# Kernel optimization log

Hardware: AMD Instinct MI355X
Metric: run time of the kernel (lower is better)

Reference implementation:

```python
import jax, jax.numpy as jnp
import numpy as np

EPS = 1e-7  # keras_backend.epsilon()
ROUTINGS = 3


def setup_inputs() -> dict:
    key = jax.random.key(0)
    k1, k2, k3, k4, k5 = jax.random.split(key, 5)
    B, H, W, I, O = 32, 8, 8, 32, 64
    return {
        "inputs_poses": jax.random.normal(k1, (B, H, W, I, 4, 4), dtype=jnp.float32),
        "inputs_activations": jax.random.uniform(k2, (B, H, W, I), dtype=jnp.float32),
        "w": jax.random.normal(k3, (I, O, 4, 4), dtype=jnp.float32),
        "beta_v": jax.random.normal(k4, (1, O), dtype=jnp.float32),
        "beta_a": jax.random.normal(k5, (1, O), dtype=jnp.float32),
    }


def _em_routing(votes, i_act, beta_v, beta_a, routings):
    # votes: [B, N, O, 16], i_act: [B, N]
    B, N, O, P = votes.shape
    act = i_act[..., None, None]              # [B, N, 1, 1]
    bv = beta_v[..., None, :, None]           # [1, 1, O, 1]
    ba = beta_a[..., None, :, None]           # [1, 1, O, 1]
    rr = jnp.full((N, O, 1), 1.0 / O, dtype=votes.dtype)
    it_min, it_max = 1.0, min(routings, 3.0)
    o_mean = o_act = None
    for it in range(routings):
        inv_temp = it_min + (it_max - it_min) * it / max(1.0, routings - 1.0)
        # ---- m-step ----
        rr_prime = rr * act                                    # [B, N, O, 1]
        rps = rr_prime.sum(axis=-3, keepdims=True)             # [B, 1, O, 1]
        o_mean = (rr_prime * votes).sum(axis=-3, keepdims=True) / rps   # [B,1,O,16]
        o_stdv = jnp.sqrt((rr_prime * jnp.square(votes - o_mean)).sum(axis=-3, keepdims=True) / rps)
        o_cost_h = (bv + jnp.log(o_stdv + EPS)) * rps          # [B,1,O,16]
        o_cost = o_cost_h.sum(axis=-1, keepdims=True)          # [B,1,O,1]
        o_cost_mean = o_cost.mean(axis=-2, keepdims=True)      # [B,1,1,1]
        o_cost_stdv = jnp.sqrt(jnp.square(o_cost - o_cost_mean).sum(axis=-2, keepdims=True) / O)
        o_act = jax.nn.sigmoid(inv_temp * (ba + (o_cost_mean - o_cost) / (o_cost_stdv + EPS)))
        # ---- e-step ----
        if it < routings - 1:
            o_p = (-jnp.sum(jnp.square(votes - o_mean) / (2.0 * jnp.square(o_stdv)), axis=-1, keepdims=True)
                   - jnp.sum(jnp.log(o_stdv + EPS), axis=-1, keepdims=True))   # [B,N,O,1]
            zz = jnp.log(o_act + EPS) + o_p
            rr = jax.nn.softmax(zz, axis=-2)                   # softmax over O
    poses = jnp.squeeze(o_mean, axis=-3)                       # [B, O, 16]
    activations = jnp.squeeze(o_act, axis=(-3, -1))            # [B, O]
    return poses, activations


def reference(inputs_poses, inputs_activations, w, beta_v, beta_a):
    B, H, W, I = inputs_activations.shape
    O = w.shape[1]
    # mat_transform: per-(input-type, class) 4x4 pose transform -> votes
    pose = inputs_poses.reshape(B * H * W, I, 4, 4)
    votes = jnp.einsum('siab,iobc->sioac', pose, w)            # [BHW, I, O, 4, 4]
    votes = votes.reshape(B, H, W, I, O, 16)
    # coord_addition: add scaled spatial coords to components 0 (h) and 1 (w)
    ch = jnp.zeros((1, H, 1, 1, 1, 16), votes.dtype).at[..., 0].set(
        ((jnp.arange(H, dtype=votes.dtype) + 0.5) / H).reshape(1, H, 1, 1, 1))
    cw = jnp.zeros((1, 1, W, 1, 1, 16), votes.dtype).at[..., 1].set(
        ((jnp.arange(W, dtype=votes.dtype) + 0.5) / W).reshape(1, 1, W, 1, 1))
    votes = votes + ch + cw
    votes = votes.reshape(B, H * W * I, O, 16)
    i_act = inputs_activations.reshape(B, H * W * I)
    poses, activations = _em_routing(votes, i_act, beta_v, beta_a, ROUTINGS)
    poses = poses.reshape(B, O, 4, 4)
    return poses, activations
```

## Files before the change

### kernel.cpp

```cpp
#include <hip/hip_runtime.h>


#define NB 32
#define NN 2048
#define NO 64
#define NP 16
#define EPSF 1e-7f

#define CHUNKS 64
#define CHN 32

#define ACC_SLOTS 33
#define ACC_PER_B (ACC_SLOTS * NO)
#define ACC_TOTAL (NB * ACC_PER_B)

template <bool FIRST>
__global__ __launch_bounds__(256) void accum_kernel(
    const float* __restrict__ pose,
    const float* __restrict__ act,
    const float* __restrict__ wmat,
    const float* __restrict__ beta_v,
    const float* __restrict__ beta_a,
    const float* __restrict__ accum_prev,
    float* __restrict__ accum_out,
    float inv_temp)
{
    __shared__ float pose_s[CHN * 16];
    __shared__ float act_s[CHN];
    __shared__ float red[2][ACC_PER_B];

    const int b = blockIdx.y;
    const int site = blockIdx.x;
    const int n0 = site * CHN;
    const int tid = threadIdx.x;

    {
        const float4* psrc = (const float4*)(pose + ((size_t)b * NN + n0) * 16);
        float4* pdst = (float4*)pose_s;
        if (tid < CHN * 4) pdst[tid] = psrc[tid];
        if (tid < CHN) act_s[tid] = act[(size_t)b * NN + n0 + tid];
    }
    __syncthreads();

    const int wv = tid >> 6;
    const int o = tid & 63;

    float i2v[16], Bp[16], zzc = 0.f;
    if (!FIRST) {
        const float* ap = accum_prev + (size_t)b * ACC_PER_B;
        float rps = ap[32 * 64 + o];
        float rinv = 1.0f / rps;
        float logsum = 0.f, msum = 0.f;
        #pragma unroll
        for (int p = 0; p < 16; p++) {
            float mm = ap[p * 64 + o] * rinv;
            float vv = fmaxf(ap[(16 + p) * 64 + o] * rinv - mm * mm, 0.f);
            float iv = 0.5f / vv;
            i2v[p] = iv;
            Bp[p] = 2.0f * mm * iv;
            msum = fmaf(mm * mm, iv, msum);
            logsum += __logf(sqrtf(vv) + EPSF);
        }
        float cost = rps * (16.0f * beta_v[o] + logsum);
        float cm = cost;
        #pragma unroll
        for (int s = 32; s > 0; s >>= 1) cm += __shfl_xor(cm, s, 64);
        cm *= (1.0f / 64.0f);
        float dd = cost - cm;
        float cs = dd * dd;
        #pragma unroll
        for (int s = 32; s > 0; s >>= 1) cs += __shfl_xor(cs, s, 64);
        cs = sqrtf(cs * (1.0f / 64.0f));
        float x = inv_temp * (beta_a[o] + (cm - cost) / (cs + EPSF));
        float oa = 1.0f / (1.0f + __expf(-x));
        zzc = __logf(oa + EPSF) - logsum - msum;
    }

    const float c0 = ((site >> 3) + 0.5f) * 0.125f;
    const float c1 = ((site & 7) + 0.5f) * 0.125f;

    float accR = 0.f, acc1[16], acc2[16];
    #pragma unroll
    for (int p = 0; p < 16; p++) { acc1[p] = 0.f; acc2[p] = 0.f; }

    for (int ii = 0; ii < 8; ii++) {
        const int i = wv * 8 + ii;
        const float4* wp = (const float4*)(wmat + ((size_t)i * 64 + o) * 16);
        float4 w0 = wp[0], w1 = wp[1], w2 = wp[2], w3 = wp[3];
        const float* pr = pose_s + i * 16;
        float v[16];
        #pragma unroll
        for (int a = 0; a < 4; a++) {
            float pa0 = pr[a * 4 + 0], pa1 = pr[a * 4 + 1];
            float pa2 = pr[a * 4 + 2], pa3 = pr[a * 4 + 3];
            v[a * 4 + 0] = pa0 * w0.x + pa1 * w1.x + pa2 * w2.x + pa3 * w3.x;
            v[a * 4 + 1] = pa0 * w0.y + pa1 * w1.y + pa2 * w2.y + pa3 * w3.y;
            v[a * 4 + 2] = pa0 * w0.z + pa1 * w1.z + pa2 * w2.z + pa3 * w3.z;
            v[a * 4 + 3] = pa0 * w0.w + pa1 * w1.w + pa2 * w2.w + pa3 * w3.w;
        }
        v[0] += c0;
        v[1] += c1;

        float rr;
        if (FIRST) {
            rr = 1.0f / 64.0f;
        } else {
            float d = zzc;
            #pragma unroll
            for (int p = 0; p < 16; p++) {
                float inner = fmaf(-v[p], i2v[p], Bp[p]);
                d = fmaf(v[p], inner, d);
            }
            float mx = d;
            #pragma unroll
            for (int s = 32; s > 0; s >>= 1) mx = fmaxf(mx, __shfl_xor(mx, s, 64));
            float e = __expf(d - mx);
            float sum = e;
            #pragma unroll
            for (int s = 32; s > 0; s >>= 1) sum += __shfl_xor(sum, s, 64);
            rr = __fdividef(e, sum);
        }
        float rp = rr * act_s[i];
        accR += rp;
        #pragma unroll
        for (int p = 0; p < 16; p++) {
            acc1[p] += rp * v[p];
            acc2[p] += rp * v[p] * v[p];
        }
    }

    if (wv >= 2) {
        float* r = red[wv - 2];
        r[32 * 64 + o] = accR;
        #pragma unroll
        for (int p = 0; p < 16; p++) r[p * 64 + o] = acc1[p];
        #pragma unroll
        for (int p = 0; p < 16; p++) r[(16 + p) * 64 + o] = acc2[p];
    }
    __syncthreads();
    if (wv < 2) {
        const float* r = red[wv];
        accR += r[32 * 64 + o];
        #pragma unroll
        for (int p = 0; p < 16; p++) acc1[p] += r[p * 64 + o];
        #pragma unroll
        for (int p = 0; p < 16; p++) acc2[p] += r[(16 + p) * 64 + o];
    }
    __syncthreads();
    if (wv == 1) {
        float* r = red[0];
        r[32 * 64 + o] = accR;
        #pragma unroll
        for (int p = 0; p < 16; p++) r[p * 64 + o] = acc1[p];
        #pragma unroll
        for (int p = 0; p < 16; p++) r[(16 + p) * 64 + o] = acc2[p];
    }
    __syncthreads();
    if (wv == 0) {
        const float* r = red[0];
        accR += r[32 * 64 + o];
        #pragma unroll
        for (int p = 0; p < 16; p++) acc1[p] += r[p * 64 + o];
        #pragma unroll
        for (int p = 0; p < 16; p++) acc2[p] += r[(16 + p) * 64 + o];

        float* ac = accum_out + (size_t)b * ACC_PER_B;
        atomicAdd(ac + 32 * 64 + o, accR);
        #pragma unroll
        for (int p = 0; p < 16; p++) atomicAdd(ac + p * 64 + o, acc1[p]);
        #pragma unroll
        for (int p = 0; p < 16; p++) atomicAdd(ac + (16 + p) * 64 + o, acc2[p]);
    }
}

__global__ __launch_bounds__(64) void stats_final(
    const float* __restrict__ accum,
    const float* __restrict__ beta_v,
    const float* __restrict__ beta_a,
    float* __restrict__ out,
    float inv_temp)
{
    const int b = blockIdx.x;
    const int o = threadIdx.x;
    const float* ac = accum + (size_t)b * ACC_PER_B;

    float rps = ac[32 * 64 + o];
    float rinv = 1.0f / rps;
    float m[16];
    float logsum = 0.f;
    #pragma unroll
    for (int p = 0; p < 16; p++) {
        float mm = ac[p * 64 + o] * rinv;
        float vv = fmaxf(ac[(16 + p) * 64 + o] * rinv - mm * mm, 0.f);
        m[p] = mm;
        logsum += __logf(sqrtf(vv) + EPSF);
    }
    float cost = rps * (16.0f * beta_v[o] + logsum);

    float cm = cost;
    #pragma unroll
    for (int s = 32; s > 0; s >>= 1) cm += __shfl_xor(cm, s, 64);
    cm *= (1.0f / 64.0f);
    float dd = cost - cm;
    float cs = dd * dd;
    #pragma unroll
    for (int s = 32; s > 0; s >>= 1) cs += __shfl_xor(cs, s, 64);
    cs = sqrtf(cs * (1.0f / 64.0f));

    float x = inv_temp * (beta_a[o] + (cm - cost) / (cs + EPSF));
    float oa = 1.0f / (1.0f + __expf(-x));

    float* op = out + ((size_t)b * 64 + o) * 16;
    #pragma unroll
    for (int p = 0; p < 16; p++) op[p] = m[p];
    out[(size_t)NB * NO * NP + (size_t)b * 64 + o] = oa;
}

extern "C" void kernel_launch(void* const* d_in, const int* in_sizes, int n_in,
                              void* d_out, int out_size, void* d_ws, size_t ws_size,
                              hipStream_t stream) {
    const float* pose   = (const float*)d_in[0];
    const float* act    = (const float*)d_in[1];
    const float* wmat   = (const float*)d_in[2];
    const float* beta_v = (const float*)d_in[3];
    const float* beta_a = (const float*)d_in[4];
    float* out = (float*)d_out;
    float* ws = (float*)d_ws;

    float* a0 = ws;
    float* a1 = ws + (size_t)ACC_TOTAL;
    float* a2 = ws + 2 * (size_t)ACC_TOTAL;

    hipMemsetAsync(ws, 0, 3 * (size_t)ACC_TOTAL * sizeof(float), stream);

    dim3 grid(CHUNKS, NB);
    accum_kernel<true ><<<grid, 256, 0, stream>>>(pose, act, wmat, beta_v, beta_a,
                                                  nullptr, a0, 0.0f);
    accum_kernel<false><<<grid, 256, 0, stream>>>(pose, act, wmat, beta_v, beta_a,
                                                  a0, a1, 1.0f);
    accum_kernel<false><<<grid, 256, 0, stream>>>(pose, act, wmat, beta_v, beta_a,
                                                  a1, a2, 2.0f);
    stats_final<<<NB, 64, 0, stream>>>(a2, beta_v, beta_a, out, 3.0f);
}
```

Baseline: 173.1 us.

## Retile accumulation blocks by site group and input type to hoist weight loads

Each block now covers 8 spatial sites by 4 input types instead of one site by all 32 input types. Every wave then owns one fixed input type and loads its 4x4 weight row once, instead of reloading weights for each of its 8 iterations. The shared-memory pose/activation staging is gathered with a strided index pattern and overlapped with the previous-iteration stats computation before the barrier. The e-step log-likelihood is rewritten in the direct (v-m)^2 form, and the fast divide is swapped for a regular divide, which adds a few instructions per iteration but may improve numerical accuracy.

```diff
diff --git a/kernel.cpp b/kernel.cpp
--- a/kernel.cpp
+++ b/kernel.cpp
@@ -7,8 +7,9 @@
 #define NP 16
 #define EPSF 1e-7f
 
-#define CHUNKS 64
-#define CHN 32
+#define SITES_PB 8
+#define IS_PB 4
+#define PAIRS_PB (SITES_PB * IS_PB)
 
 #define ACC_SLOTS 33
 #define ACC_PER_B (ACC_SLOTS * NO)
@@ -25,40 +26,48 @@
     float* __restrict__ accum_out,
     float inv_temp)
 {
-    __shared__ float pose_s[CHN * 16];
-    __shared__ float act_s[CHN];
+    __shared__ float pose_s[PAIRS_PB * 16];
+    __shared__ float act_s[PAIRS_PB];
     __shared__ float red[2][ACC_PER_B];
 
     const int b = blockIdx.y;
-    const int site = blockIdx.x;
-    const int n0 = site * CHN;
+    const int sg = blockIdx.x >> 3;
+    const int ig = blockIdx.x & 7;
+    const int s0 = sg * SITES_PB;
+    const int i0 = ig * IS_PB;
     const int tid = threadIdx.x;
-
-    {
-        const float4* psrc = (const float4*)(pose + ((size_t)b * NN + n0) * 16);
-        float4* pdst = (float4*)pose_s;
-        if (tid < CHN * 4) pdst[tid] = psrc[tid];
-        if (tid < CHN) act_s[tid] = act[(size_t)b * NN + n0 + tid];
-    }
-    __syncthreads();
-
     const int wv = tid >> 6;
     const int o = tid & 63;
 
-    float i2v[16], Bp[16], zzc = 0.f;
+    {
+        if (tid < PAIRS_PB * 4) {
+            const int pair = tid >> 2, qw = tid & 3;
+            const int sl = pair >> 2, li = pair & 3;
+            const size_t n = (size_t)b * NN + (s0 + sl) * 32 + (i0 + li);
+            ((float4*)pose_s)[pair * 4 + qw] =
+                ((const float4*)(pose + n * 16))[qw];
+        }
+        if (tid < PAIRS_PB) {
+            const int sl = tid >> 2, li = tid & 3;
+            act_s[tid] = act[(size_t)b * NN + (s0 + sl) * 32 + (i0 + li)];
+        }
+    }
+
+    const float4* wp = (const float4*)(wmat + (((size_t)(i0 + wv)) * 64 + o) * 16);
+    float4 w0 = wp[0], w1 = wp[1], w2 = wp[2], w3 = wp[3];
+
+    float m[16], i2v[16], zzb = 0.f;
     if (!FIRST) {
         const float* ap = accum_prev + (size_t)b * ACC_PER_B;
         float rps = ap[32 * 64 + o];
         float rinv = 1.0f / rps;
-        float logsum = 0.f, msum = 0.f;
+        float logsum = 0.f;
         #pragma unroll
         for (int p = 0; p < 16; p++) {
             float mm = ap[p * 64 + o] * rinv;
             float vv = fmaxf(ap[(16 + p) * 64 + o] * rinv - mm * mm, 0.f);
-            float iv = 0.5f / vv;
-            i2v[p] = iv;
-            Bp[p] = 2.0f * mm * iv;
-            msum = fmaf(mm * mm, iv, msum);
+            m[p] = mm;
+            i2v[p] = 0.5f / vv;
             logsum += __logf(sqrtf(vv) + EPSF);
         }
         float cost = rps * (16.0f * beta_v[o] + logsum);
@@ -73,21 +82,20 @@
         cs = sqrtf(cs * (1.0f / 64.0f));
         float x = inv_temp * (beta_a[o] + (cm - cost) / (cs + EPSF));
         float oa = 1.0f / (1.0f + __expf(-x));
-        zzc = __logf(oa + EPSF) - logsum - msum;
-    }
-
-    const float c0 = ((site >> 3) + 0.5f) * 0.125f;
-    const float c1 = ((site & 7) + 0.5f) * 0.125f;
+        zzb = __logf(oa + EPSF) - logsum;
+    }
+    __syncthreads();
 
     float accR = 0.f, acc1[16], acc2[16];
     #pragma unroll
     for (int p = 0; p < 16; p++) { acc1[p] = 0.f; acc2[p] = 0.f; }
 
-    for (int ii = 0; ii < 8; ii++) {
-        const int i = wv * 8 + ii;
-        const float4* wp = (const float4*)(wmat + ((size_t)i * 64 + o) * 16);
-        float4 w0 = wp[0], w1 = wp[1], w2 = wp[2], w3 = wp[3];
-        const float* pr = pose_s + i * 16;
+    for (int sl = 0; sl < 8; sl++) {
+        const int site = s0 + sl;
+        const float c0 = ((site >> 3) + 0.5f) * 0.125f;
+        const float c1 = ((site & 7) + 0.5f) * 0.125f;
+        const float* pr = pose_s + (sl * 4 + wv) * 16;
+
         float v[16];
         #pragma unroll
         for (int a = 0; a < 4; a++) {
@@ -105,11 +113,11 @@
         if (FIRST) {
             rr = 1.0f / 64.0f;
         } else {
-            float d = zzc;
+            float d = zzb;
             #pragma unroll
             for (int p = 0; p < 16; p++) {
-                float inner = fmaf(-v[p], i2v[p], Bp[p]);
-                d = fmaf(v[p], inner, d);
+                float t = v[p] - m[p];
+                d -= t * t * i2v[p];
             }
             float mx = d;
             #pragma unroll
@@ -118,9 +126,9 @@
             float sum = e;
             #pragma unroll
             for (int s = 32; s > 0; s >>= 1) sum += __shfl_xor(sum, s, 64);
-            rr = __fdividef(e, sum);
-        }
-        float rp = rr * act_s[i];
+            rr = e / sum;
+        }
+        float rp = rr * act_s[sl * 4 + wv];
         accR += rp;
         #pragma unroll
         for (int p = 0; p < 16; p++) {
@@ -233,7 +241,7 @@
 
     hipMemsetAsync(ws, 0, 3 * (size_t)ACC_TOTAL * sizeof(float), stream);
 
-    dim3 grid(CHUNKS, NB);
+    dim3 grid(64, NB);
     accum_kernel<true ><<<grid, 256, 0, stream>>>(pose, act, wmat, beta_v, beta_a,
                                                   nullptr, a0, 0.0f);
     accum_kernel<false><<<grid, 256, 0, stream>>>(pose, act, wmat, beta_v, beta_a,
```

After: 165.1 us. -4.7%, faster.
